# Performance work log

Hardware: AMD Instinct MI355X
Metric: run time of the kernel (lower is better)

Reference implementation:

```python
import jax, jax.numpy as jnp
import numpy as np

N_A, N_B = 30000, 30000
V, D_IN, D_OUT, H, E = 2, 128, 128, 4, 480000
EPS_LN = 1e-5


def setup_inputs() -> dict:
    key = jax.random.key(0)
    ks = jax.random.split(key, 22)
    rn = lambda i, sh, s=1.0: jax.random.normal(ks[i], sh, dtype=jnp.float32) * s
    ri = lambda i, n: jax.random.randint(ks[i], (E,), 0, n, dtype=jnp.int32)
    return {
        'feat_A': rn(0, (N_A, V, D_IN)),
        'feat_B': rn(1, (N_B, V, D_IN)),
        'src_ab': ri(2, N_A), 'dst_ab': ri(3, N_B),
        'val_ab': jax.random.uniform(ks[4], (E,), dtype=jnp.float32),
        'src_ba': ri(5, N_B), 'dst_ba': ri(6, N_A),
        'val_ba': jax.random.uniform(ks[7], (E,), dtype=jnp.float32),
        'W1': rn(8, (D_OUT, D_IN), 0.05), 'b1': jnp.zeros((D_OUT,), jnp.float32),
        'g1': jnp.ones((D_OUT,), jnp.float32), 'be1': jnp.zeros((D_OUT,), jnp.float32),
        'W2': rn(9, (D_OUT, D_IN), 0.05), 'b2': jnp.zeros((D_OUT,), jnp.float32),
        'g2': jnp.ones((D_OUT,), jnp.float32), 'be2': jnp.zeros((D_OUT,), jnp.float32),
        'Win': rn(10, (3 * D_OUT, D_OUT), 0.05), 'bin_': jnp.zeros((3 * D_OUT,), jnp.float32),
        'Wout': rn(11, (D_OUT, D_OUT), 0.05), 'bout': jnp.zeros((D_OUT,), jnp.float32),
        'lng': jnp.ones((D_OUT,), jnp.float32), 'lnb': jnp.zeros((D_OUT,), jnp.float32),
    }


def spmm_t(src, dst, val, h, n_out):
    # (adj^T @ h) over all views: h [N_src, V, d] -> [n_out, V, d]
    msg = h[src] * val[:, None, None]
    return jax.ops.segment_sum(msg, dst, num_segments=n_out)


def l2norm(x):
    n = jnp.sqrt(jnp.sum(x * x, axis=-1, keepdims=True))
    return x / jnp.maximum(n, 1e-12)


def layernorm(x, g, b):
    mu = jnp.mean(x, axis=-1, keepdims=True)
    var = jnp.mean((x - mu) ** 2, axis=-1, keepdims=True)
    return (x - mu) * jax.lax.rsqrt(var + EPS_LN) * g + b


def proj(x, W, b, g, be):
    # Linear -> LayerNorm -> ReLU
    return jax.nn.relu(layernorm(x @ W.T + b, g, be))


def mha(x, Win, bin_, Wout, bout, num_heads):
    # self-attention over the metapath axis P; x [..., P, d]
    *lead, P, d = x.shape
    dh = d // num_heads
    q, k, v = jnp.split(x @ Win.T + bin_, 3, axis=-1)
    hd = lambda t: t.reshape(*lead, P, num_heads, dh)
    q = hd(q) * (dh ** -0.5)
    scores = jnp.einsum('...qhe,...khe->...hqk', q, hd(k))
    a = jax.nn.softmax(scores, axis=-1)
    o = jnp.einsum('...hqk,...khe->...qhe', a, hd(v)).reshape(*lead, P, d)
    return o @ Wout.T + bout


def reference(feat_A, feat_B, src_ab, dst_ab, val_ab, src_ba, dst_ba, val_ba,
              W1, b1, g1, be1, W2, b2, g2, be2, Win, bin_, Wout, bout, lng, lnb):
    # metapath A->B->A
    h = l2norm(spmm_t(src_ab, dst_ab, val_ab, feat_A, N_B))
    h = l2norm(spmm_t(src_ba, dst_ba, val_ba, h, N_A))
    h1 = proj(h, W1, b1, g1, be1)                       # [N_A, V, d]
    # metapath B->A
    h = l2norm(spmm_t(src_ba, dst_ba, val_ba, feat_B, N_A))
    h2 = proj(h, W2, b2, g2, be2)                       # [N_A, V, d]
    x = jnp.stack([h1, h2], axis=2)                     # [N_A, V, P=2, d]
    attn = mha(x, Win, bin_, Wout, bout, H)
    y = layernorm(attn + x, lng, lnb).mean(axis=2)      # [N_A, V, d]
    return y  # h_global['A']; type B is identity passthrough of feat_B
```

## Files before the change

### kernel.cpp

```cpp
#include <hip/hip_runtime.h>

#define D 128
#define NODE_ROW 256
#define AP 8
#define AR (AP * 2)

typedef __attribute__((ext_vector_type(8))) short short8;
typedef __attribute__((ext_vector_type(4))) float floatx4;

__device__ __forceinline__ ushort f2bf(float f) {
    unsigned int u = __float_as_uint(f);
    u += 0x7fffu + ((u >> 16) & 1u);
    return (ushort)(u >> 16);
}
__device__ __forceinline__ unsigned int pk2(float a, float b) {
    return (unsigned int)f2bf(a) | ((unsigned int)f2bf(b) << 16);
}
__device__ __forceinline__ void up8(uint4 u, float* f) {
    f[0] = __uint_as_float(u.x << 16); f[1] = __uint_as_float(u.x & 0xffff0000u);
    f[2] = __uint_as_float(u.y << 16); f[3] = __uint_as_float(u.y & 0xffff0000u);
    f[4] = __uint_as_float(u.z << 16); f[5] = __uint_as_float(u.z & 0xffff0000u);
    f[6] = __uint_as_float(u.w << 16); f[7] = __uint_as_float(u.w & 0xffff0000u);
}
__device__ __forceinline__ float bf2f(ushort h) {
    return __uint_as_float(((unsigned int)h) << 16);
}
__device__ __forceinline__ short8 ldfrag(const ushort* p) {
    union { uint4 u; short8 s; } cv;
    cv.u = *(const uint4*)p;
    return cv.s;
}
__device__ __forceinline__ void acc4(float4& a, float w, uint2 u) {
    a.x += w * __uint_as_float(u.x << 16);
    a.y += w * __uint_as_float(u.x & 0xffff0000u);
    a.z += w * __uint_as_float(u.y << 16);
    a.w += w * __uint_as_float(u.y & 0xffff0000u);
}

__global__ __launch_bounds__(256) void k_f2b2(
    const float* __restrict__ srcA, const float* __restrict__ srcB,
    ushort* __restrict__ dstA, ushort* __restrict__ dstB, int n8) {
    int i = blockIdx.x * 256 + threadIdx.x;
    const float* s; ushort* d; int k;
    if (i < n8) { s = srcA; d = dstA; k = i; }
    else if (i < 2 * n8) { s = srcB; d = dstB; k = i - n8; }
    else return;
    const float4* sp = (const float4*)s + (size_t)k * 2;
    float4 a = sp[0], b = sp[1];
    uint4 o;
    o.x = pk2(a.x, a.y); o.y = pk2(a.z, a.w);
    o.z = pk2(b.x, b.y); o.w = pk2(b.z, b.w);
    ((uint4*)d)[k] = o;
}


__global__ __launch_bounds__(256) void k_hist(
    const int* __restrict__ dst_ab, const int* __restrict__ dst_ba,
    int* __restrict__ cnt_ab, int* __restrict__ cnt_ba, int E) {
    int i = blockIdx.x * 256 + threadIdx.x;
    if (i >= E) return;
    atomicAdd(&cnt_ab[dst_ab[i]], 1);
    atomicAdd(&cnt_ba[dst_ba[i]], 1);
}

__global__ __launch_bounds__(1024) void k_scan2(
    int* __restrict__ cntB, int* __restrict__ startB, int nB_,
    int* __restrict__ cntA, int* __restrict__ startA, int nA_) {
    __shared__ int part[1024];
    int* cnt; int* start; int n;
    if (blockIdx.x == 0) { cnt = cntB; start = startB; n = nB_; }
    else                 { cnt = cntA; start = startA; n = nA_; }
    int t = threadIdx.x;
    int chunk = (n + 1023) >> 10;
    int lo = min(t * chunk, n), hi = min(lo + chunk, n);
    int s = 0;
    for (int i = lo; i < hi; i++) s += cnt[i];
    part[t] = s;
    __syncthreads();
    for (int d = 1; d < 1024; d <<= 1) {
        int v = (t >= d) ? part[t - d] : 0;
        __syncthreads();
        part[t] += v;
        __syncthreads();
    }
    int off = part[t] - s;
    for (int i = lo; i < hi; i++) {
        int c = cnt[i];
        start[i] = off;
        cnt[i] = off;
        off += c;
    }
    if (t == 1023) start[n] = off;
}

__global__ __launch_bounds__(256) void k_scatter(
    const int* __restrict__ src_ab, const int* __restrict__ dst_ab,
    const float* __restrict__ val_ab,
    const int* __restrict__ src_ba, const int* __restrict__ dst_ba,
    const float* __restrict__ val_ba,
    int* __restrict__ cur_ab, int* __restrict__ cur_ba,
    int2* __restrict__ ep_ab, int2* __restrict__ ep_ba, int E) {
    int i = blockIdx.x * 256 + threadIdx.x;
    if (i >= E) return;
    {
        int pos = atomicAdd(&cur_ab[dst_ab[i]], 1);
        ep_ab[pos] = make_int2(src_ab[i], __float_as_int(val_ab[i]));
    }
    {
        int pos = atomicAdd(&cur_ba[dst_ba[i]], 1);
        ep_ba[pos] = make_int2(src_ba[i], __float_as_int(val_ba[i]));
    }
}


__global__ __launch_bounds__(256) void k_gather_norm_bf(
    const ushort* __restrict__ feat, const int2* __restrict__ ep,
    const int* __restrict__ start, ushort* __restrict__ out, int n) {
    int node = blockIdx.x * 4 + (threadIdx.x >> 6);
    if (node >= n) return;
    int lane = threadIdx.x & 63;
    int lo = start[node], hi = start[node + 1];
    float4 acc = make_float4(0.f, 0.f, 0.f, 0.f);
    int i = lo;
    for (; i + 3 < hi; i += 4) {
        int2 p0 = ep[i], p1 = ep[i + 1], p2 = ep[i + 2], p3 = ep[i + 3];
        uint2 u0 = ((const uint2*)(feat + (size_t)p0.x * NODE_ROW))[lane];
        uint2 u1 = ((const uint2*)(feat + (size_t)p1.x * NODE_ROW))[lane];
        uint2 u2 = ((const uint2*)(feat + (size_t)p2.x * NODE_ROW))[lane];
        uint2 u3 = ((const uint2*)(feat + (size_t)p3.x * NODE_ROW))[lane];
        acc4(acc, __int_as_float(p0.y), u0);
        acc4(acc, __int_as_float(p1.y), u1);
        acc4(acc, __int_as_float(p2.y), u2);
        acc4(acc, __int_as_float(p3.y), u3);
    }
    for (; i < hi; i++) {
        int2 p = ep[i];
        uint2 u = ((const uint2*)(feat + (size_t)p.x * NODE_ROW))[lane];
        acc4(acc, __int_as_float(p.y), u);
    }
    float ss = acc.x * acc.x + acc.y * acc.y + acc.z * acc.z + acc.w * acc.w;
    #pragma unroll
    for (int o = 16; o > 0; o >>= 1) ss += __shfl_xor(ss, o, 32);
    float sc = 1.0f / fmaxf(sqrtf(ss), 1e-12f);
    uint2 o;
    o.x = pk2(acc.x * sc, acc.y * sc);
    o.y = pk2(acc.z * sc, acc.w * sc);
    ((uint2*)(out + (size_t)node * NODE_ROW))[lane] = o;
}

__global__ __launch_bounds__(256) void k_gather2_bf(
    const ushort* __restrict__ featP, const ushort* __restrict__ featQ,
    const int2* __restrict__ ep, const int* __restrict__ start,
    ushort* __restrict__ outP, ushort* __restrict__ outQ, int n) {
    int node = blockIdx.x * 4 + (threadIdx.x >> 6);
    if (node >= n) return;
    int lane = threadIdx.x & 63;
    int lo = start[node], hi = start[node + 1];
    float4 aP = make_float4(0.f, 0.f, 0.f, 0.f);
    float4 aQ = make_float4(0.f, 0.f, 0.f, 0.f);
    int i = lo;
    for (; i + 3 < hi; i += 4) {
        int2 p0 = ep[i], p1 = ep[i + 1], p2 = ep[i + 2], p3 = ep[i + 3];
        size_t o0 = (size_t)p0.x * NODE_ROW, o1 = (size_t)p1.x * NODE_ROW;
        size_t o2 = (size_t)p2.x * NODE_ROW, o3 = (size_t)p3.x * NODE_ROW;
        uint2 uP0 = ((const uint2*)(featP + o0))[lane];
        uint2 uQ0 = ((const uint2*)(featQ + o0))[lane];
        uint2 uP1 = ((const uint2*)(featP + o1))[lane];
        uint2 uQ1 = ((const uint2*)(featQ + o1))[lane];
        uint2 uP2 = ((const uint2*)(featP + o2))[lane];
        uint2 uQ2 = ((const uint2*)(featQ + o2))[lane];
        uint2 uP3 = ((const uint2*)(featP + o3))[lane];
        uint2 uQ3 = ((const uint2*)(featQ + o3))[lane];
        float w0 = __int_as_float(p0.y), w1 = __int_as_float(p1.y);
        float w2 = __int_as_float(p2.y), w3 = __int_as_float(p3.y);
        acc4(aP, w0, uP0); acc4(aQ, w0, uQ0);
        acc4(aP, w1, uP1); acc4(aQ, w1, uQ1);
        acc4(aP, w2, uP2); acc4(aQ, w2, uQ2);
        acc4(aP, w3, uP3); acc4(aQ, w3, uQ3);
    }
    for (; i < hi; i++) {
        int2 p = ep[i];
        float w = __int_as_float(p.y);
        size_t off = (size_t)p.x * NODE_ROW;
        uint2 uP = ((const uint2*)(featP + off))[lane];
        uint2 uQ = ((const uint2*)(featQ + off))[lane];
        acc4(aP, w, uP); acc4(aQ, w, uQ);
    }
    uint2 oP, oQ;
    oP.x = pk2(aP.x, aP.y); oP.y = pk2(aP.z, aP.w);
    oQ.x = pk2(aQ.x, aQ.y); oQ.y = pk2(aQ.z, aQ.w);
    ((uint2*)(outP + (size_t)node * NODE_ROW))[lane] = oP;
    ((uint2*)(outQ + (size_t)node * NODE_ROW))[lane] = oQ;
}

__global__ __launch_bounds__(256) void k_cvt(
    const float* __restrict__ W1, const float* __restrict__ W2,
    const float* __restrict__ Win, const float* __restrict__ Wout,
    ushort* __restrict__ dst) {
    int idx = (blockIdx.x * 256 + threadIdx.x) * 4;
    if (idx >= 98304) return;
    const float* s; int off;
    if (idx < 16384)      { s = W1;  off = idx; }
    else if (idx < 32768) { s = W2;  off = idx - 16384; }
    else if (idx < 81920) { s = Win; off = idx - 32768; }
    else                  { s = Wout; off = idx - 81920; }
    float4 f = *(const float4*)(s + off);
    uint2 p;
    p.x = pk2(f.x, f.y);
    p.y = pk2(f.z, f.w);
    *(uint2*)(dst + idx) = p;
}

__global__ __launch_bounds__(128) void k_projm2(
    const ushort* __restrict__ in1, const ushort* __restrict__ Wb1,
    const float* __restrict__ b1, const float* __restrict__ g1,
    const float* __restrict__ be1,
    const ushort* __restrict__ in2, const ushort* __restrict__ Wb2,
    const float* __restrict__ b2, const float* __restrict__ g2,
    const float* __restrict__ be2,
    ushort* __restrict__ xbuf) {
    __shared__ ushort xn[16][136];
    __shared__ float yb[16][128];
    int p = blockIdx.y;
    const ushort* in = p ? in2 : in1;
    const ushort* Wb = p ? Wb2 : Wb1;
    const float*  b  = p ? b2  : b1;
    const float*  g  = p ? g2  : g1;
    const float*  be = p ? be2 : be1;
    int t = threadIdx.x;
    size_t rowbase = (size_t)blockIdx.x * 16;
    int r = t >> 3, i = t & 7;

    {
        const ushort* gp = in + (rowbase + r) * D + i * 16;
        float v[16];
        up8(((const uint4*)gp)[0], v);
        up8(((const uint4*)gp)[1], v + 8);
        float ss = 0.f;
        #pragma unroll
        for (int e = 0; e < 16; e++) ss += v[e] * v[e];
        ss += __shfl_xor(ss, 1, 8);
        ss += __shfl_xor(ss, 2, 8);
        ss += __shfl_xor(ss, 4, 8);
        float sc = 1.0f / fmaxf(sqrtf(ss), 1e-12f);
        uint4 w0, w1;
        w0.x = pk2(v[0]*sc, v[1]*sc);   w0.y = pk2(v[2]*sc, v[3]*sc);
        w0.z = pk2(v[4]*sc, v[5]*sc);   w0.w = pk2(v[6]*sc, v[7]*sc);
        w1.x = pk2(v[8]*sc, v[9]*sc);   w1.y = pk2(v[10]*sc, v[11]*sc);
        w1.z = pk2(v[12]*sc, v[13]*sc); w1.w = pk2(v[14]*sc, v[15]*sc);
        ushort* dst = &xn[r][i * 16];
        ((uint4*)dst)[0] = w0;
        ((uint4*)dst)[1] = w1;
    }
    __syncthreads();

    {
        int lane = t & 63, w = t >> 6, c = lane & 15, quad = lane >> 4;
        short8 af[4];
        #pragma unroll
        for (int kt = 0; kt < 4; kt++)
            af[kt] = ldfrag(&xn[c][kt * 32 + quad * 8]);
        #pragma unroll
        for (int nt2 = 0; nt2 < 4; nt2++) {
            int j = (w * 4 + nt2) * 16 + c;
            floatx4 acc = {0.f, 0.f, 0.f, 0.f};
            #pragma unroll
            for (int kt = 0; kt < 4; kt++) {
                short8 bfr = ldfrag(Wb + (size_t)j * 128 + kt * 32 + quad * 8);
                acc = __builtin_amdgcn_mfma_f32_16x16x32_bf16(af[kt], bfr, acc, 0, 0, 0);
            }
            float bj = b[j];
            #pragma unroll
            for (int rg = 0; rg < 4; rg++)
                yb[quad * 4 + rg][j] = acc[rg] + bj;
        }
    }
    __syncthreads();

    {
        float v[16];
        const float* yr = &yb[r][i * 16];
        #pragma unroll
        for (int e = 0; e < 16; e++) v[e] = yr[e];
        float s1 = 0.f, s2 = 0.f;
        #pragma unroll
        for (int e = 0; e < 16; e++) { s1 += v[e]; s2 += v[e] * v[e]; }
        s1 += __shfl_xor(s1, 1, 8); s2 += __shfl_xor(s2, 1, 8);
        s1 += __shfl_xor(s1, 2, 8); s2 += __shfl_xor(s2, 2, 8);
        s1 += __shfl_xor(s1, 4, 8); s2 += __shfl_xor(s2, 4, 8);
        float mu = s1 * (1.0f / 128.0f);
        float var = s2 * (1.0f / 128.0f) - mu * mu;
        float rs = rsqrtf(var + 1e-5f);
        const float* gg = g + i * 16;
        const float* bb = be + i * 16;
        float res[16];
        #pragma unroll
        for (int e = 0; e < 16; e++)
            res[e] = fmaxf((v[e] - mu) * rs * gg[e] + bb[e], 0.f);
        ushort* op = xbuf + ((rowbase + r) * 2 + p) * D + i * 16;
        uint4 w0, w1;
        w0.x = pk2(res[0], res[1]);   w0.y = pk2(res[2], res[3]);
        w0.z = pk2(res[4], res[5]);   w0.w = pk2(res[6], res[7]);
        w1.x = pk2(res[8], res[9]);   w1.y = pk2(res[10], res[11]);
        w1.z = pk2(res[12], res[13]); w1.w = pk2(res[14], res[15]);
        ((uint4*)op)[0] = w0;
        ((uint4*)op)[1] = w1;
    }
}

__global__ __launch_bounds__(256, 6) void k_attn2(
    const ushort* __restrict__ xbuf,
    const ushort* __restrict__ Winb, const float* __restrict__ binq,
    const ushort* __restrict__ Woutb, const float* __restrict__ bout,
    const float* __restrict__ lng, const float* __restrict__ lnb,
    float* __restrict__ out) {
    __shared__ ushort xb[AR][136];
    __shared__ ushort obuf[AR][140];
    __shared__ float yy[AR][132];
    __shared__ float mu_s[AR], rs_s[AR];
    int t = threadIdx.x;
    int lane = t & 63, w = t >> 6;
    int c = lane & 15, quad = lane >> 4;
    size_t pairbase = (size_t)blockIdx.x * AP;
    size_t rowbase = pairbase * 2;

    const uint2* gx = (const uint2*)(xbuf + rowbase * D);
    #pragma unroll
    for (int i = t; i < AR * D / 4; i += 256) {
        int r = i >> 5;
        int col = (i & 31) * 4;
        *(uint2*)&xb[r][col] = gx[i];
    }
    __syncthreads();

    {
        short8 af[4];
        #pragma unroll
        for (int kt = 0; kt < 4; kt++)
            af[kt] = ldfrag(&xb[c][kt * 32 + quad * 8]);
        floatx4 aq0 = {0.f,0.f,0.f,0.f}, aq1 = {0.f,0.f,0.f,0.f};
        floatx4 ak0 = {0.f,0.f,0.f,0.f}, ak1 = {0.f,0.f,0.f,0.f};
        floatx4 av0 = {0.f,0.f,0.f,0.f}, av1 = {0.f,0.f,0.f,0.f};
        int jb = w * 32 + c;
        #pragma unroll
        for (int kt = 0; kt < 4; kt++) {
            const ushort* wp = Winb + kt * 32 + quad * 8;
            short8 f0 = ldfrag(wp + (size_t)(jb)       * 128);
            short8 f1 = ldfrag(wp + (size_t)(jb + 16)  * 128);
            short8 f2 = ldfrag(wp + (size_t)(jb + 128) * 128);
            short8 f3 = ldfrag(wp + (size_t)(jb + 144) * 128);
            short8 f4 = ldfrag(wp + (size_t)(jb + 256) * 128);
            short8 f5 = ldfrag(wp + (size_t)(jb + 272) * 128);
            aq0 = __builtin_amdgcn_mfma_f32_16x16x32_bf16(af[kt], f0, aq0, 0, 0, 0);
            aq1 = __builtin_amdgcn_mfma_f32_16x16x32_bf16(af[kt], f1, aq1, 0, 0, 0);
            ak0 = __builtin_amdgcn_mfma_f32_16x16x32_bf16(af[kt], f2, ak0, 0, 0, 0);
            ak1 = __builtin_amdgcn_mfma_f32_16x16x32_bf16(af[kt], f3, ak1, 0, 0, 0);
            av0 = __builtin_amdgcn_mfma_f32_16x16x32_bf16(af[kt], f4, av0, 0, 0, 0);
            av1 = __builtin_amdgcn_mfma_f32_16x16x32_bf16(af[kt], f5, av1, 0, 0, 0);
        }
        const float qs = 0.17677669529663687f;
        float bq0 = binq[jb] ;        float bq1 = binq[jb + 16];
        float bk0 = binq[jb + 128];   float bk1 = binq[jb + 144];
        float bv0 = binq[jb + 256];   float bv1 = binq[jb + 272];
        #pragma unroll
        for (int rg = 0; rg < 4; rg++) {
            aq0[rg] = (aq0[rg] + bq0) * qs;
            aq1[rg] = (aq1[rg] + bq1) * qs;
            ak0[rg] += bk0;  ak1[rg] += bk1;
            av0[rg] += bv0;  av1[rg] += bv1;
        }
        #pragma unroll
        for (int pl = 0; pl < 2; pl++) {
            int r0 = 2 * pl, r1 = 2 * pl + 1;
            float p00 = aq0[r0] * ak0[r0] + aq1[r0] * ak1[r0];
            float p01 = aq0[r0] * ak0[r1] + aq1[r0] * ak1[r1];
            float p10 = aq0[r1] * ak0[r0] + aq1[r1] * ak1[r0];
            float p11 = aq0[r1] * ak0[r1] + aq1[r1] * ak1[r1];
            #pragma unroll
            for (int m = 1; m < 16; m <<= 1) {
                p00 += __shfl_xor(p00, m, 16);
                p01 += __shfl_xor(p01, m, 16);
                p10 += __shfl_xor(p10, m, 16);
                p11 += __shfl_xor(p11, m, 16);
            }
            float mx0 = fmaxf(p00, p01), mx1 = fmaxf(p10, p11);
            float e00 = __expf(p00 - mx0), e01 = __expf(p01 - mx0);
            float e10 = __expf(p10 - mx1), e11 = __expf(p11 - mx1);
            float i0 = 1.f / (e00 + e01), i1 = 1.f / (e10 + e11);
            float a00 = e00 * i0, a01 = e01 * i0;
            float a10 = e10 * i1, a11 = e11 * i1;
            float o00 = a00 * av0[r0] + a01 * av0[r1];
            float o10 = a10 * av0[r0] + a11 * av0[r1];
            float o01 = a00 * av1[r0] + a01 * av1[r1];
            float o11 = a10 * av1[r0] + a11 * av1[r1];
            int row0 = quad * 4 + r0, row1 = quad * 4 + r1;
            obuf[row0][jb]      = f2bf(o00);
            obuf[row1][jb]      = f2bf(o10);
            obuf[row0][jb + 16] = f2bf(o01);
            obuf[row1][jb + 16] = f2bf(o11);
        }
    }
    __syncthreads();

    {
        short8 af[4];
        #pragma unroll
        for (int kt = 0; kt < 4; kt++)
            af[kt] = ldfrag(&obuf[c][kt * 32 + quad * 8]);
        #pragma unroll
        for (int nt2 = 0; nt2 < 2; nt2++) {
            int j = (w * 2 + nt2) * 16 + c;
            floatx4 acc = {0.f, 0.f, 0.f, 0.f};
            #pragma unroll
            for (int kt = 0; kt < 4; kt++) {
                short8 bfr = ldfrag(Woutb + (size_t)j * 128 + kt * 32 + quad * 8);
                acc = __builtin_amdgcn_mfma_f32_16x16x32_bf16(af[kt], bfr, acc, 0, 0, 0);
            }
            float bj = bout[j];
            #pragma unroll
            for (int rg = 0; rg < 4; rg++) {
                int row = quad * 4 + rg;
                yy[row][j] = acc[rg] + bj + bf2f(xb[row][j]);
            }
        }
    }
    __syncthreads();

    if (t < 128) {
        int r = t >> 3, i = t & 7;
        float s1 = 0.f, s2 = 0.f;
        const float* yr = &yy[r][i * 16];
        #pragma unroll
        for (int cc = 0; cc < 16; cc++) { float v = yr[cc]; s1 += v; s2 += v * v; }
        s1 += __shfl_down(s1, 4, 8); s2 += __shfl_down(s2, 4, 8);
        s1 += __shfl_down(s1, 2, 8); s2 += __shfl_down(s2, 2, 8);
        s1 += __shfl_down(s1, 1, 8); s2 += __shfl_down(s2, 1, 8);
        if (i == 0) {
            float mu = s1 / D;
            float var = s2 / D - mu * mu;
            mu_s[r] = mu; rs_s[r] = rsqrtf(var + 1e-5f);
        }
    }
    __syncthreads();

    if (t < 128) {
        int j = t;
        float gj = lng[j], bj = lnb[j];
        #pragma unroll
        for (int pp = 0; pp < AP; pp++) {
            int r0 = pp * 2, r1 = r0 + 1;
            float v0 = (yy[r0][j] - mu_s[r0]) * rs_s[r0] * gj + bj;
            float v1 = (yy[r1][j] - mu_s[r1]) * rs_s[r1] * gj + bj;
            out[(pairbase + pp) * D + j] = 0.5f * (v0 + v1);
        }
    }
}

extern "C" void kernel_launch(void* const* d_in, const int* in_sizes, int n_in,
                              void* d_out, int out_size, void* d_ws, size_t ws_size,
                              hipStream_t stream) {
    const float* feat_A = (const float*)d_in[0];
    const float* feat_B = (const float*)d_in[1];
    const int*   src_ab = (const int*)d_in[2];
    const int*   dst_ab = (const int*)d_in[3];
    const float* val_ab = (const float*)d_in[4];
    const int*   src_ba = (const int*)d_in[5];
    const int*   dst_ba = (const int*)d_in[6];
    const float* val_ba = (const float*)d_in[7];
    const float* W1 = (const float*)d_in[8];
    const float* b1 = (const float*)d_in[9];
    const float* g1 = (const float*)d_in[10];
    const float* be1 = (const float*)d_in[11];
    const float* W2 = (const float*)d_in[12];
    const float* b2 = (const float*)d_in[13];
    const float* g2 = (const float*)d_in[14];
    const float* be2 = (const float*)d_in[15];
    const float* Win = (const float*)d_in[16];
    const float* binq = (const float*)d_in[17];
    const float* Wout = (const float*)d_in[18];
    const float* bout = (const float*)d_in[19];
    const float* lng = (const float*)d_in[20];
    const float* lnb = (const float*)d_in[21];

    int E  = in_sizes[2];
    int nA = in_sizes[0] / NODE_ROW;
    int nB = in_sizes[1] / NODE_ROW;
    int rowsA = nA * 2;
    size_t nodeElems = (size_t)nA * NODE_ROW;

    ushort* fbA  = (ushort*)d_ws;
    ushort* fbB  = fbA + nodeElems;
    ushort* hB   = fbB + nodeElems;
    ushort* hA1  = hB + nodeElems;
    ushort* hA2  = hA1 + nodeElems;
    ushort* xbuf = hA2 + nodeElems;
    ushort* Wbf  = xbuf + (size_t)rowsA * 2 * D;
    ushort* W1b   = Wbf;
    ushort* W2b   = Wbf + 16384;
    ushort* Winb  = Wbf + 32768;
    ushort* Woutb = Wbf + 81920;
    int* cnt_ab   = (int*)(Wbf + 98304);
    int* cnt_ba   = cnt_ab + nB;
    int* start_ab = cnt_ba + nA;
    int* start_ba = start_ab + (nB + 1);
    uintptr_t a = (uintptr_t)(start_ba + (nA + 1));
    a = (a + 15) & ~(uintptr_t)15;
    int2* ep_ab = (int2*)a;
    int2* ep_ba = ep_ab + E;

    int egrid = (E + 255) / 256;
    int n8 = (int)(nodeElems / 8);

    k_f2b2<<<(2 * n8 + 255) / 256, 256, 0, stream>>>(feat_A, feat_B, fbA, fbB, n8);

    hipMemsetAsync(cnt_ab, 0, (size_t)(nA + nB) * sizeof(int), stream);
    k_hist<<<egrid, 256, 0, stream>>>(dst_ab, dst_ba, cnt_ab, cnt_ba, E);
    k_scan2<<<2, 1024, 0, stream>>>(cnt_ab, start_ab, nB, cnt_ba, start_ba, nA);
    k_scatter<<<egrid, 256, 0, stream>>>(src_ab, dst_ab, val_ab,
                                         src_ba, dst_ba, val_ba,
                                         cnt_ab, cnt_ba, ep_ab, ep_ba, E);

    k_cvt<<<96, 256, 0, stream>>>(W1, W2, Win, Wout, Wbf);

    k_gather_norm_bf<<<(nB + 3) / 4, 256, 0, stream>>>(fbA, ep_ab, start_ab, hB, nB);
    k_gather2_bf<<<(nA + 3) / 4, 256, 0, stream>>>(hB, fbB, ep_ba, start_ba,
                                                   hA1, hA2, nA);

    k_projm2<<<dim3(rowsA / 16, 2), 128, 0, stream>>>(hA1, W1b, b1, g1, be1,
                                                      hA2, W2b, b2, g2, be2, xbuf);
    k_attn2<<<rowsA / AP, 256, 0, stream>>>(xbuf, Winb, binq, Woutb, bout,
                                            lng, lnb, (float*)d_out);
}
```

Measured before the change: 567.9 us.

## Fuse second gather, projections, and attention into one tail kernel

Merges the dual-path gather over B->A edges, both Linear+LayerNorm+ReLU projections and the metapath attention plus final LayerNorm into a single kernel. Each block handles 8 nodes and keeps the intermediate rows in shared memory. This drops the global round trips through the hA1, hA2 and xbuf buffers and two kernel launches. In exchange it uses about 34 KB of shared memory per block under a launch bound of 4 blocks. It also couples the irregular gather phase with the MFMA phases inside the same block, which may lower occupancy and latency hiding. The grid is nA/8, so it assumes nA is divisible by 8.

```diff
diff --git a/kernel.cpp b/kernel.cpp
--- a/kernel.cpp
+++ b/kernel.cpp
@@ -2,8 +2,6 @@
 
 #define D 128
 #define NODE_ROW 256
-#define AP 8
-#define AR (AP * 2)
 
 typedef __attribute__((ext_vector_type(8))) short short8;
 typedef __attribute__((ext_vector_type(4))) float floatx4;
@@ -15,12 +13,6 @@
 }
 __device__ __forceinline__ unsigned int pk2(float a, float b) {
     return (unsigned int)f2bf(a) | ((unsigned int)f2bf(b) << 16);
-}
-__device__ __forceinline__ void up8(uint4 u, float* f) {
-    f[0] = __uint_as_float(u.x << 16); f[1] = __uint_as_float(u.x & 0xffff0000u);
-    f[2] = __uint_as_float(u.y << 16); f[3] = __uint_as_float(u.y & 0xffff0000u);
-    f[4] = __uint_as_float(u.z << 16); f[5] = __uint_as_float(u.z & 0xffff0000u);
-    f[6] = __uint_as_float(u.w << 16); f[7] = __uint_as_float(u.w & 0xffff0000u);
 }
 __device__ __forceinline__ float bf2f(ushort h) {
     return __uint_as_float(((unsigned int)h) << 16);
@@ -111,7 +103,6 @@
         ep_ba[pos] = make_int2(src_ba[i], __float_as_int(val_ba[i]));
     }
 }
-
 
 __global__ __launch_bounds__(256) void k_gather_norm_bf(
     const ushort* __restrict__ feat, const int2* __restrict__ ep,
@@ -148,51 +139,6 @@
     ((uint2*)(out + (size_t)node * NODE_ROW))[lane] = o;
 }
 
-__global__ __launch_bounds__(256) void k_gather2_bf(
-    const ushort* __restrict__ featP, const ushort* __restrict__ featQ,
-    const int2* __restrict__ ep, const int* __restrict__ start,
-    ushort* __restrict__ outP, ushort* __restrict__ outQ, int n) {
-    int node = blockIdx.x * 4 + (threadIdx.x >> 6);
-    if (node >= n) return;
-    int lane = threadIdx.x & 63;
-    int lo = start[node], hi = start[node + 1];
-    float4 aP = make_float4(0.f, 0.f, 0.f, 0.f);
-    float4 aQ = make_float4(0.f, 0.f, 0.f, 0.f);
-    int i = lo;
-    for (; i + 3 < hi; i += 4) {
-        int2 p0 = ep[i], p1 = ep[i + 1], p2 = ep[i + 2], p3 = ep[i + 3];
-        size_t o0 = (size_t)p0.x * NODE_ROW, o1 = (size_t)p1.x * NODE_ROW;
-        size_t o2 = (size_t)p2.x * NODE_ROW, o3 = (size_t)p3.x * NODE_ROW;
-        uint2 uP0 = ((const uint2*)(featP + o0))[lane];
-        uint2 uQ0 = ((const uint2*)(featQ + o0))[lane];
-        uint2 uP1 = ((const uint2*)(featP + o1))[lane];
-        uint2 uQ1 = ((const uint2*)(featQ + o1))[lane];
-        uint2 uP2 = ((const uint2*)(featP + o2))[lane];
-        uint2 uQ2 = ((const uint2*)(featQ + o2))[lane];
-        uint2 uP3 = ((const uint2*)(featP + o3))[lane];
-        uint2 uQ3 = ((const uint2*)(featQ + o3))[lane];
-        float w0 = __int_as_float(p0.y), w1 = __int_as_float(p1.y);
-        float w2 = __int_as_float(p2.y), w3 = __int_as_float(p3.y);
-        acc4(aP, w0, uP0); acc4(aQ, w0, uQ0);
-        acc4(aP, w1, uP1); acc4(aQ, w1, uQ1);
-        acc4(aP, w2, uP2); acc4(aQ, w2, uQ2);
-        acc4(aP, w3, uP3); acc4(aQ, w3, uQ3);
-    }
-    for (; i < hi; i++) {
-        int2 p = ep[i];
-        float w = __int_as_float(p.y);
-        size_t off = (size_t)p.x * NODE_ROW;
-        uint2 uP = ((const uint2*)(featP + off))[lane];
-        uint2 uQ = ((const uint2*)(featQ + off))[lane];
-        acc4(aP, w, uP); acc4(aQ, w, uQ);
-    }
-    uint2 oP, oQ;
-    oP.x = pk2(aP.x, aP.y); oP.y = pk2(aP.z, aP.w);
-    oQ.x = pk2(aQ.x, aQ.y); oQ.y = pk2(aQ.z, aQ.w);
-    ((uint2*)(outP + (size_t)node * NODE_ROW))[lane] = oP;
-    ((uint2*)(outQ + (size_t)node * NODE_ROW))[lane] = oQ;
-}
-
 __global__ __launch_bounds__(256) void k_cvt(
     const float* __restrict__ W1, const float* __restrict__ W2,
     const float* __restrict__ Win, const float* __restrict__ Wout,
@@ -211,65 +157,107 @@
     *(uint2*)(dst + idx) = p;
 }
 
-__global__ __launch_bounds__(128) void k_projm2(
-    const ushort* __restrict__ in1, const ushort* __restrict__ Wb1,
-    const float* __restrict__ b1, const float* __restrict__ g1,
-    const float* __restrict__ be1,
-    const ushort* __restrict__ in2, const ushort* __restrict__ Wb2,
-    const float* __restrict__ b2, const float* __restrict__ g2,
-    const float* __restrict__ be2,
-    ushort* __restrict__ xbuf) {
-    __shared__ ushort xn[16][136];
-    __shared__ float yb[16][128];
-    int p = blockIdx.y;
-    const ushort* in = p ? in2 : in1;
-    const ushort* Wb = p ? Wb2 : Wb1;
-    const float*  b  = p ? b2  : b1;
-    const float*  g  = p ? g2  : g1;
-    const float*  be = p ? be2 : be1;
+__global__ __launch_bounds__(256, 4) void k_tail(
+    const ushort* __restrict__ hB, const ushort* __restrict__ fbB,
+    const int2* __restrict__ ep, const int* __restrict__ start,
+    const ushort* __restrict__ W1b, const float* __restrict__ b1,
+    const float* __restrict__ g1, const float* __restrict__ be1,
+    const ushort* __restrict__ W2b, const float* __restrict__ b2,
+    const float* __restrict__ g2, const float* __restrict__ be2,
+    const ushort* __restrict__ Winb, const float* __restrict__ binq,
+    const ushort* __restrict__ Woutb, const float* __restrict__ bout,
+    const float* __restrict__ lng, const float* __restrict__ lnb,
+    float* __restrict__ out) {
+    __shared__ __align__(16) char pool[34816];
+    ushort (*xnP)[136] = (ushort(*)[136])(pool);
+    ushort (*xnQ)[136] = (ushort(*)[136])(pool + 4352);
+    ushort (*obuf)[140] = (ushort(*)[140])(pool);
+    float (*ybP)[128] = (float(*)[128])(pool + 8960);
+    float (*ybQ)[128] = (float(*)[128])(pool + 17152);
+    float (*yy)[132]  = (float(*)[132])(pool + 8960);
+    ushort (*xb)[136] = (ushort(*)[136])(pool + 25856);
+    float* mu_s = (float*)(pool + 34560);
+    float* rs_s = (float*)(pool + 34688);
+
     int t = threadIdx.x;
-    size_t rowbase = (size_t)blockIdx.x * 16;
-    int r = t >> 3, i = t & 7;
-
-    {
-        const ushort* gp = in + (rowbase + r) * D + i * 16;
-        float v[16];
-        up8(((const uint4*)gp)[0], v);
-        up8(((const uint4*)gp)[1], v + 8);
-        float ss = 0.f;
-        #pragma unroll
-        for (int e = 0; e < 16; e++) ss += v[e] * v[e];
-        ss += __shfl_xor(ss, 1, 8);
-        ss += __shfl_xor(ss, 2, 8);
-        ss += __shfl_xor(ss, 4, 8);
-        float sc = 1.0f / fmaxf(sqrtf(ss), 1e-12f);
-        uint4 w0, w1;
-        w0.x = pk2(v[0]*sc, v[1]*sc);   w0.y = pk2(v[2]*sc, v[3]*sc);
-        w0.z = pk2(v[4]*sc, v[5]*sc);   w0.w = pk2(v[6]*sc, v[7]*sc);
-        w1.x = pk2(v[8]*sc, v[9]*sc);   w1.y = pk2(v[10]*sc, v[11]*sc);
-        w1.z = pk2(v[12]*sc, v[13]*sc); w1.w = pk2(v[14]*sc, v[15]*sc);
-        ushort* dst = &xn[r][i * 16];
-        ((uint4*)dst)[0] = w0;
-        ((uint4*)dst)[1] = w1;
-    }
-    __syncthreads();
-
-    {
-        int lane = t & 63, w = t >> 6, c = lane & 15, quad = lane >> 4;
+    int lane = t & 63, w = t >> 6;
+    int c = lane & 15, quad = lane >> 4;
+    int n0 = blockIdx.x * 8;
+    size_t pairbase = (size_t)blockIdx.x * 16;
+
+    #pragma unroll
+    for (int nl = 0; nl < 2; nl++) {
+        int node = n0 + w * 2 + nl;
+        int lo = start[node], hi = start[node + 1];
+        float4 aP = make_float4(0.f, 0.f, 0.f, 0.f);
+        float4 aQ = make_float4(0.f, 0.f, 0.f, 0.f);
+        int i = lo;
+        for (; i + 3 < hi; i += 4) {
+            int2 p0 = ep[i], p1 = ep[i + 1], p2 = ep[i + 2], p3 = ep[i + 3];
+            size_t o0 = (size_t)p0.x * NODE_ROW, o1 = (size_t)p1.x * NODE_ROW;
+            size_t o2 = (size_t)p2.x * NODE_ROW, o3 = (size_t)p3.x * NODE_ROW;
+            uint2 uP0 = ((const uint2*)(hB + o0))[lane];
+            uint2 uQ0 = ((const uint2*)(fbB + o0))[lane];
+            uint2 uP1 = ((const uint2*)(hB + o1))[lane];
+            uint2 uQ1 = ((const uint2*)(fbB + o1))[lane];
+            uint2 uP2 = ((const uint2*)(hB + o2))[lane];
+            uint2 uQ2 = ((const uint2*)(fbB + o2))[lane];
+            uint2 uP3 = ((const uint2*)(hB + o3))[lane];
+            uint2 uQ3 = ((const uint2*)(fbB + o3))[lane];
+            float w0 = __int_as_float(p0.y), w1 = __int_as_float(p1.y);
+            float w2 = __int_as_float(p2.y), w3 = __int_as_float(p3.y);
+            acc4(aP, w0, uP0); acc4(aQ, w0, uQ0);
+            acc4(aP, w1, uP1); acc4(aQ, w1, uQ1);
+            acc4(aP, w2, uP2); acc4(aQ, w2, uQ2);
+            acc4(aP, w3, uP3); acc4(aQ, w3, uQ3);
+        }
+        for (; i < hi; i++) {
+            int2 p = ep[i];
+            float wv = __int_as_float(p.y);
+            size_t off = (size_t)p.x * NODE_ROW;
+            uint2 uP = ((const uint2*)(hB + off))[lane];
+            uint2 uQ = ((const uint2*)(fbB + off))[lane];
+            acc4(aP, wv, uP); acc4(aQ, wv, uQ);
+        }
+        float ssP = aP.x * aP.x + aP.y * aP.y + aP.z * aP.z + aP.w * aP.w;
+        float ssQ = aQ.x * aQ.x + aQ.y * aQ.y + aQ.z * aQ.z + aQ.w * aQ.w;
+        #pragma unroll
+        for (int o = 16; o > 0; o >>= 1) {
+            ssP += __shfl_xor(ssP, o, 32);
+            ssQ += __shfl_xor(ssQ, o, 32);
+        }
+        float scP = 1.0f / fmaxf(sqrtf(ssP), 1e-12f);
+        float scQ = 1.0f / fmaxf(sqrtf(ssQ), 1e-12f);
+        int rloc = (w * 2 + nl) * 2 + (lane >> 5);
+        int col = (lane & 31) * 4;
+        uint2 oP, oQ;
+        oP.x = pk2(aP.x * scP, aP.y * scP); oP.y = pk2(aP.z * scP, aP.w * scP);
+        oQ.x = pk2(aQ.x * scQ, aQ.y * scQ); oQ.y = pk2(aQ.z * scQ, aQ.w * scQ);
+        *(uint2*)&xnP[rloc][col] = oP;
+        *(uint2*)&xnQ[rloc][col] = oQ;
+    }
+    __syncthreads();
+
+    {
+        int set = w >> 1, wl = w & 1;
+        const ushort* Wb = set ? W2b : W1b;
+        const float* bb = set ? b2 : b1;
+        ushort (*xn)[136] = set ? xnQ : xnP;
+        float (*yb)[128] = set ? ybQ : ybP;
         short8 af[4];
         #pragma unroll
         for (int kt = 0; kt < 4; kt++)
             af[kt] = ldfrag(&xn[c][kt * 32 + quad * 8]);
         #pragma unroll
         for (int nt2 = 0; nt2 < 4; nt2++) {
-            int j = (w * 4 + nt2) * 16 + c;
+            int j = (wl * 4 + nt2) * 16 + c;
             floatx4 acc = {0.f, 0.f, 0.f, 0.f};
             #pragma unroll
             for (int kt = 0; kt < 4; kt++) {
                 short8 bfr = ldfrag(Wb + (size_t)j * 128 + kt * 32 + quad * 8);
                 acc = __builtin_amdgcn_mfma_f32_16x16x32_bf16(af[kt], bfr, acc, 0, 0, 0);
             }
-            float bj = b[j];
+            float bj = bb[j];
             #pragma unroll
             for (int rg = 0; rg < 4; rg++)
                 yb[quad * 4 + rg][j] = acc[rg] + bj;
@@ -278,8 +266,13 @@
     __syncthreads();
 
     {
+        int set = t >> 7, tt = t & 127;
+        int r = tt >> 3, ii = tt & 7;
+        float (*yb)[128] = set ? ybQ : ybP;
+        const float* gg = (set ? g2 : g1) + ii * 16;
+        const float* bb = (set ? be2 : be1) + ii * 16;
         float v[16];
-        const float* yr = &yb[r][i * 16];
+        const float* yr = &yb[r][ii * 16];
         #pragma unroll
         for (int e = 0; e < 16; e++) v[e] = yr[e];
         float s1 = 0.f, s2 = 0.f;
@@ -291,13 +284,11 @@
         float mu = s1 * (1.0f / 128.0f);
         float var = s2 * (1.0f / 128.0f) - mu * mu;
         float rs = rsqrtf(var + 1e-5f);
-        const float* gg = g + i * 16;
-        const float* bb = be + i * 16;
         float res[16];
         #pragma unroll
         for (int e = 0; e < 16; e++)
             res[e] = fmaxf((v[e] - mu) * rs * gg[e] + bb[e], 0.f);
-        ushort* op = xbuf + ((rowbase + r) * 2 + p) * D + i * 16;
+        ushort* op = &xb[r * 2 + set][ii * 16];
         uint4 w0, w1;
         w0.x = pk2(res[0], res[1]);   w0.y = pk2(res[2], res[3]);
         w0.z = pk2(res[4], res[5]);   w0.w = pk2(res[6], res[7]);
@@ -306,136 +297,119 @@
         ((uint4*)op)[0] = w0;
         ((uint4*)op)[1] = w1;
     }
-}
-
-__global__ __launch_bounds__(256, 6) void k_attn2(
-    const ushort* __restrict__ xbuf,
-    const ushort* __restrict__ Winb, const float* __restrict__ binq,
-    const ushort* __restrict__ Woutb, const float* __restrict__ bout,
-    const float* __restrict__ lng, const float* __restrict__ lnb,
-    float* __restrict__ out) {
-    __shared__ ushort xb[AR][136];
-    __shared__ ushort obuf[AR][140];
-    __shared__ float yy[AR][132];
-    __shared__ float mu_s[AR], rs_s[AR];
-    int t = threadIdx.x;
-    int lane = t & 63, w = t >> 6;
-    int c = lane & 15, quad = lane >> 4;
-    size_t pairbase = (size_t)blockIdx.x * AP;
-    size_t rowbase = pairbase * 2;
-
-    const uint2* gx = (const uint2*)(xbuf + rowbase * D);
-    #pragma unroll
-    for (int i = t; i < AR * D / 4; i += 256) {
-        int r = i >> 5;
-        int col = (i & 31) * 4;
-        *(uint2*)&xb[r][col] = gx[i];
-    }
-    __syncthreads();
-
-    {
-        short8 af[4];
-        #pragma unroll
-        for (int kt = 0; kt < 4; kt++)
-            af[kt] = ldfrag(&xb[c][kt * 32 + quad * 8]);
-        floatx4 aq0 = {0.f,0.f,0.f,0.f}, aq1 = {0.f,0.f,0.f,0.f};
-        floatx4 ak0 = {0.f,0.f,0.f,0.f}, ak1 = {0.f,0.f,0.f,0.f};
-        floatx4 av0 = {0.f,0.f,0.f,0.f}, av1 = {0.f,0.f,0.f,0.f};
-        int jb = w * 32 + c;
-        #pragma unroll
-        for (int kt = 0; kt < 4; kt++) {
-            const ushort* wp = Winb + kt * 32 + quad * 8;
-            short8 f0 = ldfrag(wp + (size_t)(jb)       * 128);
-            short8 f1 = ldfrag(wp + (size_t)(jb + 16)  * 128);
-            short8 f2 = ldfrag(wp + (size_t)(jb + 128) * 128);
-            short8 f3 = ldfrag(wp + (size_t)(jb + 144) * 128);
-            short8 f4 = ldfrag(wp + (size_t)(jb + 256) * 128);
-            short8 f5 = ldfrag(wp + (size_t)(jb + 272) * 128);
-            aq0 = __builtin_amdgcn_mfma_f32_16x16x32_bf16(af[kt], f0, aq0, 0, 0, 0);
-            aq1 = __builtin_amdgcn_mfma_f32_16x16x32_bf16(af[kt], f1, aq1, 0, 0, 0);
-            ak0 = __builtin_amdgcn_mfma_f32_16x16x32_bf16(af[kt], f2, ak0, 0, 0, 0);
-            ak1 = __builtin_amdgcn_mfma_f32_16x16x32_bf16(af[kt], f3, ak1, 0, 0, 0);
-            av0 = __builtin_amdgcn_mfma_f32_16x16x32_bf16(af[kt], f4, av0, 0, 0, 0);
-            av1 = __builtin_amdgcn_mfma_f32_16x16x32_bf16(af[kt], f5, av1, 0, 0, 0);
-        }
+    __syncthreads();
+
+    int jb = w * 32 + c;
+    {
         const float qs = 0.17677669529663687f;
-        float bq0 = binq[jb] ;        float bq1 = binq[jb + 16];
+        float bq0 = binq[jb];         float bq1 = binq[jb + 16];
         float bk0 = binq[jb + 128];   float bk1 = binq[jb + 144];
         float bv0 = binq[jb + 256];   float bv1 = binq[jb + 272];
         #pragma unroll
-        for (int rg = 0; rg < 4; rg++) {
-            aq0[rg] = (aq0[rg] + bq0) * qs;
-            aq1[rg] = (aq1[rg] + bq1) * qs;
-            ak0[rg] += bk0;  ak1[rg] += bk1;
-            av0[rg] += bv0;  av1[rg] += bv1;
-        }
-        #pragma unroll
-        for (int pl = 0; pl < 2; pl++) {
-            int r0 = 2 * pl, r1 = 2 * pl + 1;
-            float p00 = aq0[r0] * ak0[r0] + aq1[r0] * ak1[r0];
-            float p01 = aq0[r0] * ak0[r1] + aq1[r0] * ak1[r1];
-            float p10 = aq0[r1] * ak0[r0] + aq1[r1] * ak1[r0];
-            float p11 = aq0[r1] * ak0[r1] + aq1[r1] * ak1[r1];
-            #pragma unroll
-            for (int m = 1; m < 16; m <<= 1) {
-                p00 += __shfl_xor(p00, m, 16);
-                p01 += __shfl_xor(p01, m, 16);
-                p10 += __shfl_xor(p10, m, 16);
-                p11 += __shfl_xor(p11, m, 16);
+        for (int hf = 0; hf < 2; hf++) {
+            int rb = hf * 16;
+            short8 af[4];
+            #pragma unroll
+            for (int kt = 0; kt < 4; kt++)
+                af[kt] = ldfrag(&xb[rb + c][kt * 32 + quad * 8]);
+            floatx4 aq0 = {0.f,0.f,0.f,0.f}, aq1 = {0.f,0.f,0.f,0.f};
+            floatx4 ak0 = {0.f,0.f,0.f,0.f}, ak1 = {0.f,0.f,0.f,0.f};
+            floatx4 av0 = {0.f,0.f,0.f,0.f}, av1 = {0.f,0.f,0.f,0.f};
+            #pragma unroll
+            for (int kt = 0; kt < 4; kt++) {
+                const ushort* wp = Winb + kt * 32 + quad * 8;
+                short8 f0 = ldfrag(wp + (size_t)(jb)       * 128);
+                short8 f1 = ldfrag(wp + (size_t)(jb + 16)  * 128);
+                short8 f2 = ldfrag(wp + (size_t)(jb + 128) * 128);
+                short8 f3 = ldfrag(wp + (size_t)(jb + 144) * 128);
+                short8 f4 = ldfrag(wp + (size_t)(jb + 256) * 128);
+                short8 f5 = ldfrag(wp + (size_t)(jb + 272) * 128);
+                aq0 = __builtin_amdgcn_mfma_f32_16x16x32_bf16(af[kt], f0, aq0, 0, 0, 0);
+                aq1 = __builtin_amdgcn_mfma_f32_16x16x32_bf16(af[kt], f1, aq1, 0, 0, 0);
+                ak0 = __builtin_amdgcn_mfma_f32_16x16x32_bf16(af[kt], f2, ak0, 0, 0, 0);
+                ak1 = __builtin_amdgcn_mfma_f32_16x16x32_bf16(af[kt], f3, ak1, 0, 0, 0);
+                av0 = __builtin_amdgcn_mfma_f32_16x16x32_bf16(af[kt], f4, av0, 0, 0, 0);
+                av1 = __builtin_amdgcn_mfma_f32_16x16x32_bf16(af[kt], f5, av1, 0, 0, 0);
             }
-            float mx0 = fmaxf(p00, p01), mx1 = fmaxf(p10, p11);
-            float e00 = __expf(p00 - mx0), e01 = __expf(p01 - mx0);
-            float e10 = __expf(p10 - mx1), e11 = __expf(p11 - mx1);
-            float i0 = 1.f / (e00 + e01), i1 = 1.f / (e10 + e11);
-            float a00 = e00 * i0, a01 = e01 * i0;
-            float a10 = e10 * i1, a11 = e11 * i1;
-            float o00 = a00 * av0[r0] + a01 * av0[r1];
-            float o10 = a10 * av0[r0] + a11 * av0[r1];
-            float o01 = a00 * av1[r0] + a01 * av1[r1];
-            float o11 = a10 * av1[r0] + a11 * av1[r1];
-            int row0 = quad * 4 + r0, row1 = quad * 4 + r1;
-            obuf[row0][jb]      = f2bf(o00);
-            obuf[row1][jb]      = f2bf(o10);
-            obuf[row0][jb + 16] = f2bf(o01);
-            obuf[row1][jb + 16] = f2bf(o11);
-        }
-    }
-    __syncthreads();
-
-    {
-        short8 af[4];
-        #pragma unroll
-        for (int kt = 0; kt < 4; kt++)
-            af[kt] = ldfrag(&obuf[c][kt * 32 + quad * 8]);
-        #pragma unroll
-        for (int nt2 = 0; nt2 < 2; nt2++) {
-            int j = (w * 2 + nt2) * 16 + c;
-            floatx4 acc = {0.f, 0.f, 0.f, 0.f};
-            #pragma unroll
-            for (int kt = 0; kt < 4; kt++) {
-                short8 bfr = ldfrag(Woutb + (size_t)j * 128 + kt * 32 + quad * 8);
-                acc = __builtin_amdgcn_mfma_f32_16x16x32_bf16(af[kt], bfr, acc, 0, 0, 0);
+            #pragma unroll
+            for (int rg = 0; rg < 4; rg++) {
+                aq0[rg] = (aq0[rg] + bq0) * qs;
+                aq1[rg] = (aq1[rg] + bq1) * qs;
+                ak0[rg] += bk0;  ak1[rg] += bk1;
+                av0[rg] += bv0;  av1[rg] += bv1;
             }
-            float bj = bout[j];
-            #pragma unroll
-            for (int rg = 0; rg < 4; rg++) {
-                int row = quad * 4 + rg;
-                yy[row][j] = acc[rg] + bj + bf2f(xb[row][j]);
+            #pragma unroll
+            for (int pl = 0; pl < 2; pl++) {
+                int r0 = 2 * pl, r1 = 2 * pl + 1;
+                float p00 = aq0[r0] * ak0[r0] + aq1[r0] * ak1[r0];
+                float p01 = aq0[r0] * ak0[r1] + aq1[r0] * ak1[r1];
+                float p10 = aq0[r1] * ak0[r0] + aq1[r1] * ak1[r0];
+                float p11 = aq0[r1] * ak0[r1] + aq1[r1] * ak1[r1];
+                #pragma unroll
+                for (int m = 1; m < 16; m <<= 1) {
+                    p00 += __shfl_xor(p00, m, 16);
+                    p01 += __shfl_xor(p01, m, 16);
+                    p10 += __shfl_xor(p10, m, 16);
+                    p11 += __shfl_xor(p11, m, 16);
+                }
+                float mx0 = fmaxf(p00, p01), mx1 = fmaxf(p10, p11);
+                float e00 = __expf(p00 - mx0), e01 = __expf(p01 - mx0);
+                float e10 = __expf(p10 - mx1), e11 = __expf(p11 - mx1);
+                float i0 = 1.f / (e00 + e01), i1 = 1.f / (e10 + e11);
+                float a00 = e00 * i0, a01 = e01 * i0;
+                float a10 = e10 * i1, a11 = e11 * i1;
+                float o00 = a00 * av0[r0] + a01 * av0[r1];
+                float o10 = a10 * av0[r0] + a11 * av0[r1];
+                float o01 = a00 * av1[r0] + a01 * av1[r1];
+                float o11 = a10 * av1[r0] + a11 * av1[r1];
+                int row0 = rb + quad * 4 + r0, row1 = rb + quad * 4 + r1;
+                obuf[row0][jb]      = f2bf(o00);
+                obuf[row1][jb]      = f2bf(o10);
+                obuf[row0][jb + 16] = f2bf(o01);
+                obuf[row1][jb + 16] = f2bf(o11);
             }
         }
     }
     __syncthreads();
 
-    if (t < 128) {
-        int r = t >> 3, i = t & 7;
+    {
+        #pragma unroll
+        for (int hf = 0; hf < 2; hf++) {
+            int rb = hf * 16;
+            short8 af[4];
+            #pragma unroll
+            for (int kt = 0; kt < 4; kt++)
+                af[kt] = ldfrag(&obuf[rb + c][kt * 32 + quad * 8]);
+            #pragma unroll
+            for (int nt2 = 0; nt2 < 2; nt2++) {
+                int j = (w * 2 + nt2) * 16 + c;
+                floatx4 acc = {0.f, 0.f, 0.f, 0.f};
+                #pragma unroll
+                for (int kt = 0; kt < 4; kt++) {
+                    short8 bfr = ldfrag(Woutb + (size_t)j * 128 + kt * 32 + quad * 8);
+                    acc = __builtin_amdgcn_mfma_f32_16x16x32_bf16(af[kt], bfr, acc, 0, 0, 0);
+                }
+                float bj = bout[j];
+                #pragma unroll
+                for (int rg = 0; rg < 4; rg++) {
+                    int row = rb + quad * 4 + rg;
+                    yy[row][j] = acc[rg] + bj + bf2f(xb[row][j]);
+                }
+            }
+        }
+    }
+    __syncthreads();
+
+    {
+        int r = t >> 3, ii = t & 7;
         float s1 = 0.f, s2 = 0.f;
-        const float* yr = &yy[r][i * 16];
+        const float* yr = &yy[r][ii * 16];
         #pragma unroll
         for (int cc = 0; cc < 16; cc++) { float v = yr[cc]; s1 += v; s2 += v * v; }
         s1 += __shfl_down(s1, 4, 8); s2 += __shfl_down(s2, 4, 8);
         s1 += __shfl_down(s1, 2, 8); s2 += __shfl_down(s2, 2, 8);
         s1 += __shfl_down(s1, 1, 8); s2 += __shfl_down(s2, 1, 8);
-        if (i == 0) {
+        if (ii == 0) {
             float mu = s1 / D;
             float var = s2 / D - mu * mu;
             mu_s[r] = mu; rs_s[r] = rsqrtf(var + 1e-5f);
@@ -447,7 +421,7 @@
         int j = t;
         float gj = lng[j], bj = lnb[j];
         #pragma unroll
-        for (int pp = 0; pp < AP; pp++) {
+        for (int pp = 0; pp < 16; pp++) {
             int r0 = pp * 2, r1 = r0 + 1;
             float v0 = (yy[r0][j] - mu_s[r0]) * rs_s[r0] * gj + bj;
             float v1 = (yy[r1][j] - mu_s[r1]) * rs_s[r1] * gj + bj;
@@ -491,9 +465,9 @@
     ushort* fbA  = (ushort*)d_ws;
     ushort* fbB  = fbA + nodeElems;
     ushort* hB   = fbB + nodeElems;
-    ushort* hA1  = hB + nodeElems;
-    ushort* hA2  = hA1 + nodeElems;
-    ushort* xbuf = hA2 + nodeElems;
+    ushort* hA1  = hB + nodeElems;      (void)hA1;
+    ushort* hA2  = hA1 + nodeElems;     (void)hA2;
+    ushort* xbuf = hA2 + nodeElems;     (void)xbuf;
     ushort* Wbf  = xbuf + (size_t)rowsA * 2 * D;
     ushort* W1b   = Wbf;
     ushort* W2b   = Wbf + 16384;
@@ -523,11 +497,10 @@
     k_cvt<<<96, 256, 0, stream>>>(W1, W2, Win, Wout, Wbf);
 
     k_gather_norm_bf<<<(nB + 3) / 4, 256, 0, stream>>>(fbA, ep_ab, start_ab, hB, nB);
-    k_gather2_bf<<<(nA + 3) / 4, 256, 0, stream>>>(hB, fbB, ep_ba, start_ba,
-                                                   hA1, hA2, nA);
-
-    k_projm2<<<dim3(rowsA / 16, 2), 128, 0, stream>>>(hA1, W1b, b1, g1, be1,
-                                                      hA2, W2b, b2, g2, be2, xbuf);
-    k_attn2<<<rowsA / AP, 256, 0, stream>>>(xbuf, Winb, binq, Woutb, bout,
-                                            lng, lnb, (float*)d_out);
-}
+
+    k_tail<<<nA / 8, 256, 0, stream>>>(hB, fbB, ep_ba, start_ba,
+                                       W1b, b1, g1, be1,
+                                       W2b, b2, g2, be2,
+                                       Winb, binq, Woutb, bout,
+                                       lng, lnb, (float*)d_out);
+}
```

Result: faster. 546.3 us (-3.8%).
